# Kernel optimization log

Hardware: AMD Instinct MI355X
Metric: run time of the kernel (lower is better)

## Reference

```python
import jax, jax.numpy as jnp
import numpy as np

B, C, H, W = 8, 512, 64, 64
K = 8
NUM = K * K          # number of channel groups / graph nodes
CG = C // NUM        # channels per group (8)
NC = 19              # num_classes
OUT = 512            # bottleneck out_channels


def make_dct_weight():
    # Per-channel 2D DCT basis. Channel ch belongs to group g = ch // CG;
    # group g selects frequency (u, v) = (g % K, g // K).
    g = np.arange(C) // CG
    u = (g % K).astype(np.float64)
    v = (g // K).astype(np.float64)
    th = (np.arange(H) + 0.5) / H   # [H]
    tw = (np.arange(W) + 0.5) / W   # [W]
    bh = np.cos(np.pi * u[:, None] * th[None, :])  # [C,H]
    bw = np.cos(np.pi * v[:, None] * tw[None, :])  # [C,W]
    return (bh[:, :, None] * bw[:, None, :]).astype(np.float32)  # [C,H,W]


def setup_inputs() -> dict:
    key = jax.random.key(0)
    ks = jax.random.split(key, 10)
    s = lambda i, shape: jax.random.normal(ks[i], shape, jnp.float32) * 0.05
    return {
        'x': jax.random.normal(ks[0], (B, C, H, W), jnp.float32),
        'dct_w': jnp.asarray(make_dct_weight()),
        'dm_w1': s(1, (CG, CG)),
        'dm_gamma': jnp.ones((CG,), jnp.float32),
        'dm_beta': jnp.zeros((CG,), jnp.float32),
        'dm_w2': s(2, (NC, CG)),
        'dm_b2': s(3, (NC,)),
        'fuse_w': s(4, (NUM,)),
        'fuse_b': s(5, (1,)),
        'gcn_w1': s(6, (NUM, NUM)),
        'gcn_w2': s(7, (CG, CG)),
        'bot_w': s(8, (OUT, 2 * C, 3, 3)),
        'bot_gamma': jnp.ones((OUT,), jnp.float32),
        'bot_beta': jnp.zeros((OUT,), jnp.float32),
    }


def reference(x, dct_w, dm_w1, dm_gamma, dm_beta, dm_w2, dm_b2,
              fuse_w, fuse_b, gcn_w1, gcn_w2, bot_w, bot_gamma, bot_beta):
    # MultiSpectralDCTLayer: elementwise DCT basis multiply, keeps [B,C,H,W]
    fres = x * dct_w[None]

    # channel_split -> grouped layout [B, NUM, CG, H*W]
    xg = x.reshape(B, NUM, CG, H * W)
    fg = fres.reshape(B, NUM, CG, H * W)

    # decoder_map: 1x1 conv -> BN(eval, mean=0,var=1) -> ReLU -> (Dropout=id) -> 1x1 conv
    h1 = jnp.einsum('dc,bncp->bndp', dm_w1, fg)
    h1 = jax.nn.relu(h1 * dm_gamma[None, None, :, None] + dm_beta[None, None, :, None])
    fres_map = jnp.einsum('kc,bncp->bnkp', dm_w2, h1) + dm_b2[None, None, :, None]  # [B,n,NC,HW]

    # fuse: 1x1 conv over group dim n -> [B,NC,H,W]
    fres_map_output = (jnp.einsum('n,bnkp->bkp', fuse_w, fres_map) + fuse_b[0]).reshape(B, NC, H, W)

    # local frequency class centers: [B,n,NC,HW] @ [B,n,HW,c] -> [B,n,NC,c]
    fHWc = fg.transpose(0, 1, 3, 2)   # [B,n,HW,c]
    xHWc = xg.transpose(0, 1, 3, 2)   # [B,n,HW,c]
    local = jnp.einsum('bnkp,bnpc->bnkc', fres_map, fHWc)

    # GCN over n (node) dim: conv1 + residual ReLU, then Linear over c
    g = jnp.einsum('mn,bnkc->bmkc', gcn_w1, local)
    g = jax.nn.relu(g + local)
    local = jnp.einsum('bnkc,dc->bnkd', g, gcn_w2)

    # attention combine: softmax(x @ local^T) @ local
    wm = jax.nn.softmax(jnp.einsum('bnpc,bnkc->bnpk', xHWc, local), axis=-1)  # [B,n,HW,NC]
    out = jnp.einsum('bnpk,bnkc->bnpc', wm, local)  # [B,n,HW,c]

    # channel_recover -> [B,C,H,W]
    out = out.transpose(0, 1, 3, 2).reshape(B, C, H, W)

    # bottleneck: 3x3 conv on concat, BN(eval) affine, ReLU
    cat = jnp.concatenate([x, out], axis=1)  # [B,2C,H,W]
    y = jax.lax.conv_general_dilated(cat, bot_w, (1, 1), 'SAME',
                                     dimension_numbers=('NCHW', 'OIHW', 'NCHW'))
    y = jax.nn.relu(y * bot_gamma[None, :, None, None] + bot_beta[None, :, None, None])
    return (y, fres_map_output)
```

## Files before the change

### kernel.cpp

```cpp
#include <hip/hip_runtime.h>


typedef __attribute__((ext_vector_type(8))) unsigned short u16x8;
typedef __attribute__((ext_vector_type(8))) __bf16 bf16x8;
typedef __attribute__((ext_vector_type(4))) float f32x4;

__device__ inline unsigned short f2bf(float f) {
    unsigned int u = __float_as_uint(f);
    u += 0x7fffu + ((u >> 16) & 1u);
    return (unsigned short)(u >> 16);
}

__device__ inline float bf2f(unsigned short u) {
    return __uint_as_float(((unsigned int)u) << 16);
}

__device__ __forceinline__ void gload16(unsigned short* lds, const unsigned short* g) {
    __builtin_amdgcn_global_load_lds(
        (const __attribute__((address_space(1))) unsigned int*)g,
        (__attribute__((address_space(3))) unsigned int*)lds, 16, 0, 0);
}

__global__ __launch_bounds__(256) void dct_split(const float* __restrict__ dct,
                                                 float* __restrict__ bhw) {
    const int i = blockIdx.x * 256 + threadIdx.x;
    const int c = i >> 6;
    const int k = i & 63;
    bhw[i] = dct[(size_t)c * 4096 + k * 64];
    bhw[32768 + i] = dct[(size_t)c * 4096 + k] / dct[(size_t)c * 4096];
}

__global__ __launch_bounds__(256) void repack_w(const float* __restrict__ w,
                                                unsigned short* __restrict__ wt) {
    __shared__ float buf[9216];
    const int oc = blockIdx.x;
    const int tid = threadIdx.x;
    const float* src = w + (size_t)oc * 9216;
    for (int i = tid; i < 9216; i += 256) buf[i] = src[i];
    __syncthreads();
#pragma unroll
    for (int t = 0; t < 9; ++t) {
        for (int i = tid; i < 1024; i += 256)
            wt[((size_t)t * 512 + oc) * 1024 + i] = f2bf(buf[i * 9 + t]);
    }
}

__global__ __launch_bounds__(256) void front_kernel(
    const float* __restrict__ x, const float* __restrict__ bhw,
    const float* __restrict__ w1, const float* __restrict__ gamma,
    const float* __restrict__ beta, const float* __restrict__ w2,
    const float* __restrict__ b2, const float* __restrict__ fuse_w,
    float* __restrict__ part, float* __restrict__ fpart,
    unsigned short* __restrict__ cat) {
    __shared__ __align__(16) float fgs[8][260];
    __shared__ __align__(16) float fms[19][260];
    __shared__ float sw1[64], sw2[152], sb2[19], sg[8], sb[8], sfw[64];
    const int bid = blockIdx.x;
    const int sp = bid >> 7;
    const int b = (bid >> 4) & 7;
    const int ch = bid & 15;
    const int tid = threadIdx.x;
    if (tid < 64) { sw1[tid] = w1[tid]; sfw[tid] = fuse_w[tid]; }
    if (tid < 152) sw2[tid] = w2[tid];
    if (tid < 19) sb2[tid] = b2[tid];
    if (tid < 8) { sg[tid] = gamma[tid]; sb[tid] = beta[tid]; }
    __syncthreads();
    const int p = ch * 256 + tid;
    const int hh = p >> 6;
    const int ww = p & 63;
    const float* bhp = bhw;
    const float* bwp = bhw + 32768;
    const int kk = tid >> 3, cc = tid & 7;
    float facc[19];
#pragma unroll
    for (int k = 0; k < 19; ++k) facc[k] = 0.f;
    for (int nn = 0; nn < 16; ++nn) {
        const int n = sp * 16 + nn;
        float fg[8];
        u16x8 xw;
#pragma unroll
        for (int c = 0; c < 8; ++c) {
            const int chn = n * 8 + c;
            const float xv = x[((size_t)(b * 512 + chn)) * 4096 + p];
            fg[c] = xv * (bhp[chn * 64 + hh] * bwp[chn * 64 + ww]);
            xw[c] = f2bf(xv);
            fgs[c][tid] = fg[c];
        }
        *(u16x8*)(cat + ((size_t)(b * 4096) + p) * 1024 + n * 8) = xw;
        float h1[8];
#pragma unroll
        for (int d = 0; d < 8; ++d) {
            float s = 0.f;
#pragma unroll
            for (int c = 0; c < 8; ++c) s = fmaf(sw1[d * 8 + c], fg[c], s);
            h1[d] = fmaxf(fmaf(s, sg[d], sb[d]), 0.f);
        }
        const float fw = sfw[n];
#pragma unroll
        for (int k = 0; k < 19; ++k) {
            float s = sb2[k];
#pragma unroll
            for (int d = 0; d < 8; ++d) s = fmaf(sw2[k * 8 + d], h1[d], s);
            fms[k][tid] = s;
            facc[k] = fmaf(fw, s, facc[k]);
        }
        __syncthreads();
        if (tid < 152) {
            float accv = 0.f;
#pragma unroll 8
            for (int p4 = 0; p4 < 256; p4 += 4) {
                const float4 a = *(const float4*)&fms[kk][p4];
                const float4 g4 = *(const float4*)&fgs[cc][p4];
                accv += a.x * g4.x + a.y * g4.y + a.z * g4.z + a.w * g4.w;
            }
            part[((size_t)((b * 64 + n) * 16) + ch) * 152 + tid] = accv;
        }
        __syncthreads();
    }
#pragma unroll
    for (int k = 0; k < 19; ++k)
        fpart[((size_t)(sp * 8 + b) * 19 + k) * 4096 + p] = facc[k];
}

__global__ __launch_bounds__(256) void fuse_reduce(
    const float* __restrict__ fpart, const float* __restrict__ fuse_b,
    float* __restrict__ out1) {
    const int i = blockIdx.x * 256 + threadIdx.x;
    float s = fuse_b[0];
#pragma unroll
    for (int sp = 0; sp < 4; ++sp) s += fpart[(size_t)sp * 622592 + i];
    out1[i] = s;
}

__global__ __launch_bounds__(256) void lsum_kernel(
    const float* __restrict__ part, float* __restrict__ L) {
    const int i = blockIdx.x * 256 + threadIdx.x;
    const int bn = i / 152;
    const int t = i - bn * 152;
    float s = 0.f;
#pragma unroll
    for (int ch = 0; ch < 16; ++ch)
        s += part[((size_t)(bn * 16 + ch)) * 152 + t];
    L[i] = s;
}

__global__ __launch_bounds__(256) void gcn2_kernel(
    const float* __restrict__ Lg, const float* __restrict__ w1,
    const float* __restrict__ w2, float* __restrict__ local2) {
    __shared__ float L[9728];
    __shared__ float R[1216];
    __shared__ float sw1[4096];
    __shared__ float sw2[64];
    const int b = blockIdx.x >> 3;
    const int n0 = (blockIdx.x & 7) * 8;
    const int tid = threadIdx.x;
    for (int i = tid; i < 9728; i += 256) L[i] = Lg[(size_t)b * 9728 + i];
    for (int i = tid; i < 4096; i += 256) sw1[i] = w1[i];
    if (tid < 64) sw2[tid] = w2[tid];
    __syncthreads();
    for (int i = tid; i < 1216; i += 256) {
        const int nn = i / 152, t = i - nn * 152;
        const int m = n0 + nn;
        float g = 0.f;
        for (int n = 0; n < 64; ++n) g = fmaf(sw1[m * 64 + n], L[n * 152 + t], g);
        R[i] = fmaxf(g + L[m * 152 + t], 0.f);
    }
    __syncthreads();
    for (int i = tid; i < 1216; i += 256) {
        const int nn = i / 152, t = i - nn * 152;
        const int k = t >> 3, d = t & 7;
        float s = 0.f;
#pragma unroll
        for (int c = 0; c < 8; ++c) s = fmaf(R[nn * 152 + k * 8 + c], sw2[d * 8 + c], s);
        local2[(size_t)b * 9728 + (n0 + nn) * 152 + t] = s;
    }
}

__global__ __launch_bounds__(256) void attn_kernel(
    const float* __restrict__ local2, unsigned short* __restrict__ cat) {
    __shared__ float Ls[2432];
    const int bid = blockIdx.x;
    const int b = bid >> 6;
    const int chunk = (bid >> 2) & 15;
    const int nq = bid & 3;
    const int tid = threadIdx.x;
    for (int i = tid; i < 2432; i += 256)
        Ls[i] = local2[(size_t)b * 9728 + nq * 2432 + i];
    __syncthreads();
    const int p = chunk * 256 + tid;
    unsigned short* base = cat + ((size_t)(b * 4096) + p) * 1024;
#pragma unroll 4
    for (int nn = 0; nn < 16; ++nn) {
        const int n = nq * 16 + nn;
        const u16x8 xr = *(const u16x8*)(base + n * 8);
        float xv[8];
#pragma unroll
        for (int c = 0; c < 8; ++c) xv[c] = bf2f(xr[c]);
        const float* L = Ls + nn * 152;
        float lg[19];
        float mx = -1e30f;
#pragma unroll
        for (int k = 0; k < 19; ++k) {
            float s = 0.f;
#pragma unroll
            for (int c = 0; c < 8; ++c) s = fmaf(xv[c], L[k * 8 + c], s);
            lg[k] = s;
            mx = fmaxf(mx, s);
        }
        float se = 0.f;
#pragma unroll
        for (int k = 0; k < 19; ++k) {
            lg[k] = __expf(lg[k] - mx);
            se += lg[k];
        }
        const float inv = 1.f / se;
        float ov[8];
#pragma unroll
        for (int c = 0; c < 8; ++c) ov[c] = 0.f;
#pragma unroll
        for (int k = 0; k < 19; ++k) {
#pragma unroll
            for (int c = 0; c < 8; ++c) ov[c] = fmaf(lg[k], L[k * 8 + c], ov[c]);
        }
        u16x8 w;
#pragma unroll
        for (int c = 0; c < 8; ++c) w[c] = f2bf(ov[c] * inv);
        *(u16x8*)(base + 512 + n * 8) = w;
    }
}

__global__ __launch_bounds__(512, 1) void conv_kernel(
    const unsigned short* __restrict__ cat, const unsigned short* __restrict__ wt,
    const unsigned short* __restrict__ zp,
    const float* __restrict__ gamma, const float* __restrict__ beta,
    float* __restrict__ out) {
    __shared__ __align__(16) unsigned short As[10 * 4096];
    __shared__ __align__(16) unsigned short Bs[2 * 16384];
    const int bid0 = blockIdx.x;
    const int bid = (bid0 & 7) * 32 + (bid0 >> 3);
    const int mt = bid >> 1;
    const int nt = bid & 1;
    const int b = mt >> 4;
    const int pix0 = (mt & 15) * 256;
    const int y0 = (mt & 15) * 4;
    const int ocb = nt * 256;
    const int tid = threadIdx.x;
    const int w = tid >> 6;
    const int lane = tid & 63;
    const int l16 = lane & 15;
    const int khalf = lane >> 4;
    const int wr1 = w >> 2;
    const int wrow = wr1 * 64;
    const int wcol = (w & 3) * 32;
    const int sx = tid >> 3;
    const int icsw = ((tid & 7) ^ ((tid >> 3) & 7)) * 8;
    const unsigned short* zps = zp + icsw;
    const unsigned short* catb = cat + ((size_t)b * 4096) * 1024 + icsw;
    int colk[3][2];
#pragma unroll
    for (int d = 0; d < 3; ++d)
#pragma unroll
        for (int ks = 0; ks < 2; ++ks)
            colk[d][ks] = ((ks * 64 + khalf * 16) ^ (((l16 + d - 1) & 7) << 4)) >> 1;

    f32x4 acc[2][2][4][2];
#pragma unroll
    for (int qm = 0; qm < 2; ++qm)
#pragma unroll
        for (int qn = 0; qn < 2; ++qn)
#pragma unroll
            for (int m = 0; m < 4; ++m)
#pragma unroll
                for (int n = 0; n < 2; ++n)
#pragma unroll
                    for (int j = 0; j < 4; ++j) acc[qm][qn][m][n][j] = 0.f;

    bf16x8 af[4][2];
    bf16x8 bq[2][2];
    const bf16x8 zf = {};

#define AF_READ(QM, DY, DX)                                                        \
    {                                                                              \
        const int r_ = (QM) * 2 + wr1 + (DY) + 1;                                  \
        const int phys_ = (r_ < 2) ? r_ : r_ + 4 * cp;                             \
        const int rb_ = phys_ * 4096;                                              \
        _Pragma("unroll") for (int m_ = 0; m_ < 4; ++m_) {                         \
            const int xm_ = m_ * 16 + l16 + (DX);                                  \
            const int xc_ = ((DX) == 0) ? xm_ : min(max(xm_, 0), 63);              \
            const int ab_ = rb_ + xc_ * 64;                                        \
            _Pragma("unroll") for (int ks_ = 0; ks_ < 2; ++ks_)                    \
                af[m_][ks_] = *(const bf16x8*)(As + ab_ + colk[(DX) + 1][ks_]);    \
            if ((DX) == -1 && m_ == 0 && l16 == 0) { af[0][0] = zf; af[0][1] = zf; } \
            if ((DX) == 1 && m_ == 3 && l16 == 15) { af[3][0] = zf; af[3][1] = zf; } \
        }                                                                          \
    }

#define BQ_READ(SOFF, QN)                                                          \
    _Pragma("unroll") for (int n_ = 0; n_ < 2; ++n_)                               \
        _Pragma("unroll") for (int ks_ = 0; ks_ < 2; ++ks_)                        \
            bq[n_][ks_] = *(const bf16x8*)(Bs + (SOFF) +                           \
                ((QN) * 128 + wcol + n_ * 16 + l16) * 64 + colk[1][ks_]);

#define STAGE_BH(H, SWOFF, TAP, ICB)                                               \
    _Pragma("unroll") for (int j_ = 0; j_ < 2; ++j_) {                             \
        gload16(Bs + (SWOFF) + (H) * 8192 + (j_ * 512 + tid) * 8,                  \
                wt + (size_t)(TAP) * 524288 +                                      \
                    (size_t)(ocb + (H) * 128 + j_ * 64 + sx) * 1024 + (ICB) + icsw); \
    }

#define STAGE_AROW(R)                                                              \
    do {                                                                           \
        const int yy_ = y0 - 1 + (R);                                              \
        const int ph_ = ((R) < 2) ? (R) : (R) + 4 * cp1;                           \
        const unsigned short* s2_ = ((unsigned)yy_ < 64u)                          \
            ? catb + ((size_t)(yy_ * 64 + sx)) * 1024 + iccn : zps;                \
        gload16(As + ph_ * 4096 + tid * 8, s2_);                                   \
    } while (0)

#define MFMA_Q(QM, QN)                                                             \
    __builtin_amdgcn_s_setprio(1);                                                 \
    _Pragma("unroll") for (int m_ = 0; m_ < 4; ++m_)                               \
        _Pragma("unroll") for (int n_ = 0; n_ < 2; ++n_)                           \
            _Pragma("unroll") for (int ks_ = 0; ks_ < 2; ++ks_)                    \
                acc[QM][QN][m_][n_] = __builtin_amdgcn_mfma_f32_16x16x32_bf16(     \
                    af[m_][ks_], bq[n_][ks_], acc[QM][QN][m_][n_], 0, 0, 0);       \
    __builtin_amdgcn_s_setprio(0);

#define VWAIT(N)                                                                   \
    asm volatile("s_waitcnt vmcnt(" #N ")" ::: "memory");                          \
    __builtin_amdgcn_sched_barrier(0);

#define TAP_BODY(T, DY, DX, AROW, W0N, W2N)                                        \
    {                                                                              \
        const int s_ = (c + (T)) & 1;                                              \
        const int sr_ = s_ << 14;                                                  \
        const int sw_ = sr_ ^ 16384;                                               \
        const int tn_ = ((T) == 8) ? 0 : (T) + 1;                                  \
        const int icb_ = ((T) == 8) ? iccn : icc;                                  \
                                                                  \
        VWAIT(W0N)                                                                 \
        __builtin_amdgcn_s_barrier();                                              \
        __builtin_amdgcn_sched_barrier(0);                                         \
        AF_READ(0, DY, DX)                                                         \
        BQ_READ(sr_, 0)                                                            \
        STAGE_BH(0, sw_, tn_, icb_)                                                \
        MFMA_Q(0, 0)                                                               \
                                                                  \
        AF_READ(1, DY, DX)                                                         \
        if ((AROW) >= 0) STAGE_AROW(AROW);                                         \
        MFMA_Q(1, 0)                                                               \
                                                                  \
        VWAIT(W2N)                                                                 \
        BQ_READ(sr_, 1)                                                            \
        STAGE_BH(1, sw_, tn_, icb_)                                                \
        MFMA_Q(1, 1)                                                               \
                                                                  \
        AF_READ(0, DY, DX)                                                         \
        MFMA_Q(0, 1)                                                               \
    }

    {
        const int cp1 = 0, iccn = 0;
#pragma unroll
        for (int r = 0; r < 6; ++r) STAGE_AROW(r);
    }
    STAGE_BH(0, 0, 0, 0)
    STAGE_BH(1, 0, 0, 0)

    for (int c = 0; c < 16; ++c) {
        const int cp = c & 1;
        const int cp1 = cp ^ 1;
        const int icc = c << 6;
        const int iccn = ((c + 1) & 15) << 6;
        TAP_BODY(0, -1, -1, -1, 2, 2)
        TAP_BODY(1, -1, 0, -1, 2, 2)
        TAP_BODY(2, -1, 1, -1, 2, 2)
        TAP_BODY(3, 0, -1, 0, 2, 3)
        TAP_BODY(4, 0, 0, 2, 3, 3)
        TAP_BODY(5, 0, 1, 3, 3, 3)
        TAP_BODY(6, 1, -1, 1, 3, 3)
        TAP_BODY(7, 1, 0, 4, 3, 3)
        TAP_BODY(8, 1, 1, 5, 3, 3)
    }
    asm volatile("s_waitcnt vmcnt(0)" ::: "memory");

#pragma unroll
    for (int qn = 0; qn < 2; ++qn)
#pragma unroll
        for (int n = 0; n < 2; ++n) {
            const int oc = ocb + qn * 128 + wcol + n * 16 + l16;
            const float g = gamma[oc], bb = beta[oc];
#pragma unroll
            for (int qm = 0; qm < 2; ++qm)
#pragma unroll
                for (int m = 0; m < 4; ++m) {
                    const int P = qm * 128 + wrow + m * 16 + khalf * 4;
                    float4 o;
                    o.x = fmaxf(fmaf(acc[qm][qn][m][n][0], g, bb), 0.f);
                    o.y = fmaxf(fmaf(acc[qm][qn][m][n][1], g, bb), 0.f);
                    o.z = fmaxf(fmaf(acc[qm][qn][m][n][2], g, bb), 0.f);
                    o.w = fmaxf(fmaf(acc[qm][qn][m][n][3], g, bb), 0.f);
                    *(float4*)(out + ((size_t)(b * 512 + oc)) * 4096 + pix0 + P) = o;
                }
        }
#undef AF_READ
#undef BQ_READ
#undef STAGE_BH
#undef STAGE_AROW
#undef MFMA_Q
#undef VWAIT
#undef TAP_BODY
}

extern "C" void kernel_launch(void* const* d_in, const int* in_sizes, int n_in,
                              void* d_out, int out_size, void* d_ws, size_t ws_size,
                              hipStream_t stream) {
    const float* x = (const float*)d_in[0];
    const float* dct = (const float*)d_in[1];
    const float* dm_w1 = (const float*)d_in[2];
    const float* dm_g = (const float*)d_in[3];
    const float* dm_b = (const float*)d_in[4];
    const float* dm_w2 = (const float*)d_in[5];
    const float* dm_b2 = (const float*)d_in[6];
    const float* fuse_w = (const float*)d_in[7];
    const float* fuse_b = (const float*)d_in[8];
    const float* gcn_w1 = (const float*)d_in[9];
    const float* gcn_w2 = (const float*)d_in[10];
    const float* bot_w = (const float*)d_in[11];
    const float* bot_g = (const float*)d_in[12];
    const float* bot_b = (const float*)d_in[13];

    float* y = (float*)d_out;
    float* out1 = y + (size_t)8 * 512 * 4096;
    float* part = y;
    float* fpart = y + 1245184;
    float* Lbuf = y + 3735552;
    float* bhw = y + 3813376;

    char* ws = (char*)d_ws;
    const size_t CAT_BYTES = (size_t)8 * 4096 * 1024 * 2;
    const size_t WT_BYTES = (size_t)9 * 512 * 1024 * 2;
    const size_t PART_BYTES = (size_t)2048 * 152 * 4;
    const size_t L2_BYTES = (size_t)8 * 9728 * 4;
    const size_t ZP_BYTES = 4096;
    if (ws_size < CAT_BYTES + WT_BYTES + PART_BYTES + L2_BYTES + ZP_BYTES) return;

    unsigned short* cat = (unsigned short*)ws;
    unsigned short* wt = (unsigned short*)(ws + CAT_BYTES);
    float* local2 = (float*)(ws + CAT_BYTES + WT_BYTES + PART_BYTES);
    unsigned short* zp = (unsigned short*)(ws + CAT_BYTES + WT_BYTES + PART_BYTES + L2_BYTES);

    hipMemsetAsync(zp, 0, ZP_BYTES, stream);
    dct_split<<<dim3(128), dim3(256), 0, stream>>>(dct, bhw);
    front_kernel<<<dim3(512), dim3(256), 0, stream>>>(x, bhw, dm_w1, dm_g, dm_b,
                                                      dm_w2, dm_b2, fuse_w,
                                                      part, fpart, cat);
    lsum_kernel<<<dim3(304), dim3(256), 0, stream>>>(part, Lbuf);
    gcn2_kernel<<<dim3(64), dim3(256), 0, stream>>>(Lbuf, gcn_w1, gcn_w2, local2);
    fuse_reduce<<<dim3(2432), dim3(256), 0, stream>>>(fpart, fuse_b, out1);
    repack_w<<<dim3(512), dim3(256), 0, stream>>>(bot_w, wt);
    attn_kernel<<<dim3(512), dim3(256), 0, stream>>>(local2, cat);
    conv_kernel<<<dim3(256), dim3(512), 0, stream>>>(cat, wt, zp, bot_g, bot_b, y);
}
```

Before: 401.8 us.

## Double conv block to 1024 threads, halving per-wave output tile

Measured after the change: 777.8 us. +93.6%, slower.

```diff
diff --git a/kernel.cpp b/kernel.cpp
--- a/kernel.cpp
+++ b/kernel.cpp
@@ -229,7 +229,7 @@
     }
 }
 
-__global__ __launch_bounds__(512, 1) void conv_kernel(
+__global__ __launch_bounds__(1024, 4) void conv_kernel(
     const unsigned short* __restrict__ cat, const unsigned short* __restrict__ wt,
     const unsigned short* __restrict__ zp,
     const float* __restrict__ gamma, const float* __restrict__ beta,
@@ -249,10 +249,8 @@
     const int lane = tid & 63;
     const int l16 = lane & 15;
     const int khalf = lane >> 4;
-    const int wr1 = w >> 2;
-    const int wrow = wr1 * 64;
-    const int wcol = (w & 3) * 32;
-    const int sx = tid >> 3;
+    const int wrp = w >> 3;
+    const int wcp = w & 7;
     const int icsw = ((tid & 7) ^ ((tid >> 3) & 7)) * 8;
     const unsigned short* zps = zp + icsw;
     const unsigned short* catb = cat + ((size_t)b * 4096) * 1024 + icsw;
@@ -263,7 +261,7 @@
         for (int ks = 0; ks < 2; ++ks)
             colk[d][ks] = ((ks * 64 + khalf * 16) ^ (((l16 + d - 1) & 7) << 4)) >> 1;
 
-    f32x4 acc[2][2][4][2];
+    f32x4 acc[2][2][4];
 #pragma unroll
     for (int qm = 0; qm < 2; ++qm)
 #pragma unroll
@@ -271,17 +269,15 @@
 #pragma unroll
             for (int m = 0; m < 4; ++m)
 #pragma unroll
-                for (int n = 0; n < 2; ++n)
-#pragma unroll
-                    for (int j = 0; j < 4; ++j) acc[qm][qn][m][n][j] = 0.f;
+                for (int j = 0; j < 4; ++j) acc[qm][qn][m][j] = 0.f;
 
     bf16x8 af[4][2];
-    bf16x8 bq[2][2];
+    bf16x8 bq[2];
     const bf16x8 zf = {};
 
 #define AF_READ(QM, DY, DX)                                                        \
     {                                                                              \
-        const int r_ = (QM) * 2 + wr1 + (DY) + 1;                                  \
+        const int r_ = (QM) * 2 + wrp + (DY) + 1;                                  \
         const int phys_ = (r_ < 2) ? r_ : r_ + 4 * cp;                             \
         const int rb_ = phys_ * 4096;                                              \
         _Pragma("unroll") for (int m_ = 0; m_ < 4; ++m_) {                         \
@@ -296,41 +292,37 @@
     }
 
 #define BQ_READ(SOFF, QN)                                                          \
-    _Pragma("unroll") for (int n_ = 0; n_ < 2; ++n_)                               \
-        _Pragma("unroll") for (int ks_ = 0; ks_ < 2; ++ks_)                        \
-            bq[n_][ks_] = *(const bf16x8*)(Bs + (SOFF) +                           \
-                ((QN) * 128 + wcol + n_ * 16 + l16) * 64 + colk[1][ks_]);
+    _Pragma("unroll") for (int ks_ = 0; ks_ < 2; ++ks_)                            \
+        bq[ks_] = *(const bf16x8*)(Bs + (SOFF) +                                   \
+            ((QN) * 128 + wcp * 16 + l16) * 64 + colk[1][ks_]);
 
 #define STAGE_BH(H, SWOFF, TAP, ICB)                                               \
-    _Pragma("unroll") for (int j_ = 0; j_ < 2; ++j_) {                             \
-        gload16(Bs + (SWOFF) + (H) * 8192 + (j_ * 512 + tid) * 8,                  \
-                wt + (size_t)(TAP) * 524288 +                                      \
-                    (size_t)(ocb + (H) * 128 + j_ * 64 + sx) * 1024 + (ICB) + icsw); \
-    }
-
-#define STAGE_AROW(R)                                                              \
+    gload16(Bs + (SWOFF) + (H) * 8192 + tid * 8,                                   \
+            wt + (size_t)(TAP) * 524288 +                                          \
+                (size_t)(ocb + (H) * 128 + (tid >> 3)) * 1024 + (ICB) + icsw);
+
+#define STAGE_APAIR(R)                                                             \
     do {                                                                           \
-        const int yy_ = y0 - 1 + (R);                                              \
-        const int ph_ = ((R) < 2) ? (R) : (R) + 4 * cp1;                           \
+        const int yy_ = y0 - 1 + (R) + (tid >> 9);                                 \
+        const int slot_ = ((R) == 0) ? 0 : ((R) + 4 * cp1);                        \
         const unsigned short* s2_ = ((unsigned)yy_ < 64u)                          \
-            ? catb + ((size_t)(yy_ * 64 + sx)) * 1024 + iccn : zps;                \
-        gload16(As + ph_ * 4096 + tid * 8, s2_);                                   \
+            ? catb + ((size_t)(yy_ * 64 + ((tid >> 3) & 63))) * 1024 + iccn : zps; \
+        gload16(As + slot_ * 4096 + tid * 8, s2_);                                 \
     } while (0)
 
 #define MFMA_Q(QM, QN)                                                             \
     __builtin_amdgcn_s_setprio(1);                                                 \
     _Pragma("unroll") for (int m_ = 0; m_ < 4; ++m_)                               \
-        _Pragma("unroll") for (int n_ = 0; n_ < 2; ++n_)                           \
-            _Pragma("unroll") for (int ks_ = 0; ks_ < 2; ++ks_)                    \
-                acc[QM][QN][m_][n_] = __builtin_amdgcn_mfma_f32_16x16x32_bf16(     \
-                    af[m_][ks_], bq[n_][ks_], acc[QM][QN][m_][n_], 0, 0, 0);       \
+        _Pragma("unroll") for (int ks_ = 0; ks_ < 2; ++ks_)                        \
+            acc[QM][QN][m_] = __builtin_amdgcn_mfma_f32_16x16x32_bf16(             \
+                af[m_][ks_], bq[ks_], acc[QM][QN][m_], 0, 0, 0);                   \
     __builtin_amdgcn_s_setprio(0);
 
 #define VWAIT(N)                                                                   \
     asm volatile("s_waitcnt vmcnt(" #N ")" ::: "memory");                          \
     __builtin_amdgcn_sched_barrier(0);
 
-#define TAP_BODY(T, DY, DX, AROW, W0N, W2N)                                        \
+#define TAP_BODY(T, DY, DX, APAIR, W0N, W2N)                                       \
     {                                                                              \
         const int s_ = (c + (T)) & 1;                                              \
         const int sr_ = s_ << 14;                                                  \
@@ -347,7 +339,7 @@
         MFMA_Q(0, 0)                                                               \
                                                                   \
         AF_READ(1, DY, DX)                                                         \
-        if ((AROW) >= 0) STAGE_AROW(AROW);                                         \
+        if ((APAIR) >= 0) STAGE_APAIR(APAIR);                                      \
         MFMA_Q(1, 0)                                                               \
                                                                   \
         VWAIT(W2N)                                                                 \
@@ -356,13 +348,15 @@
         MFMA_Q(1, 1)                                                               \
                                                                   \
         AF_READ(0, DY, DX)                                                         \
+        BQ_READ(sr_, 1)                                                            \
         MFMA_Q(0, 1)                                                               \
     }
 
     {
         const int cp1 = 0, iccn = 0;
-#pragma unroll
-        for (int r = 0; r < 6; ++r) STAGE_AROW(r);
+        STAGE_APAIR(0);
+        STAGE_APAIR(2);
+        STAGE_APAIR(4);
     }
     STAGE_BH(0, 0, 0, 0)
     STAGE_BH(1, 0, 0, 0)
@@ -372,41 +366,39 @@
         const int cp1 = cp ^ 1;
         const int icc = c << 6;
         const int iccn = ((c + 1) & 15) << 6;
-        TAP_BODY(0, -1, -1, -1, 2, 2)
-        TAP_BODY(1, -1, 0, -1, 2, 2)
-        TAP_BODY(2, -1, 1, -1, 2, 2)
-        TAP_BODY(3, 0, -1, 0, 2, 3)
-        TAP_BODY(4, 0, 0, 2, 3, 3)
-        TAP_BODY(5, 0, 1, 3, 3, 3)
-        TAP_BODY(6, 1, -1, 1, 3, 3)
-        TAP_BODY(7, 1, 0, 4, 3, 3)
-        TAP_BODY(8, 1, 1, 5, 3, 3)
+        TAP_BODY(0, -1, -1, -1, 1, 1)
+        TAP_BODY(1, -1, 0, -1, 1, 1)
+        TAP_BODY(2, -1, 1, -1, 1, 1)
+        TAP_BODY(3, 0, -1, 2, 1, 2)
+        TAP_BODY(4, 0, 0, 4, 2, 2)
+        TAP_BODY(5, 0, 1, -1, 2, 1)
+        TAP_BODY(6, 1, -1, 0, 1, 2)
+        TAP_BODY(7, 1, 0, -1, 2, 1)
+        TAP_BODY(8, 1, 1, -1, 1, 1)
     }
     asm volatile("s_waitcnt vmcnt(0)" ::: "memory");
 
 #pragma unroll
-    for (int qn = 0; qn < 2; ++qn)
-#pragma unroll
-        for (int n = 0; n < 2; ++n) {
-            const int oc = ocb + qn * 128 + wcol + n * 16 + l16;
-            const float g = gamma[oc], bb = beta[oc];
-#pragma unroll
-            for (int qm = 0; qm < 2; ++qm)
-#pragma unroll
-                for (int m = 0; m < 4; ++m) {
-                    const int P = qm * 128 + wrow + m * 16 + khalf * 4;
-                    float4 o;
-                    o.x = fmaxf(fmaf(acc[qm][qn][m][n][0], g, bb), 0.f);
-                    o.y = fmaxf(fmaf(acc[qm][qn][m][n][1], g, bb), 0.f);
-                    o.z = fmaxf(fmaf(acc[qm][qn][m][n][2], g, bb), 0.f);
-                    o.w = fmaxf(fmaf(acc[qm][qn][m][n][3], g, bb), 0.f);
-                    *(float4*)(out + ((size_t)(b * 512 + oc)) * 4096 + pix0 + P) = o;
-                }
-        }
+    for (int qn = 0; qn < 2; ++qn) {
+        const int oc = ocb + qn * 128 + wcp * 16 + l16;
+        const float g = gamma[oc], bb = beta[oc];
+#pragma unroll
+        for (int qm = 0; qm < 2; ++qm)
+#pragma unroll
+            for (int m = 0; m < 4; ++m) {
+                const int P = qm * 128 + wrp * 64 + m * 16 + khalf * 4;
+                float4 o;
+                o.x = fmaxf(fmaf(acc[qm][qn][m][0], g, bb), 0.f);
+                o.y = fmaxf(fmaf(acc[qm][qn][m][1], g, bb), 0.f);
+                o.z = fmaxf(fmaf(acc[qm][qn][m][2], g, bb), 0.f);
+                o.w = fmaxf(fmaf(acc[qm][qn][m][3], g, bb), 0.f);
+                *(float4*)(out + ((size_t)(b * 512 + oc)) * 4096 + pix0 + P) = o;
+            }
+    }
 #undef AF_READ
 #undef BQ_READ
 #undef STAGE_BH
-#undef STAGE_AROW
+#undef STAGE_APAIR
 #undef MFMA_Q
 #undef VWAIT
 #undef TAP_BODY
@@ -460,5 +452,5 @@
     fuse_reduce<<<dim3(2432), dim3(256), 0, stream>>>(fpart, fuse_b, out1);
     repack_w<<<dim3(512), dim3(256), 0, stream>>>(bot_w, wt);
     attn_kernel<<<dim3(512), dim3(256), 0, stream>>>(local2, cat);
-    conv_kernel<<<dim3(256), dim3(512), 0, stream>>>(cat, wt, zp, bot_g, bot_b, y);
-}
+    conv_kernel<<<dim3(256), dim3(1024), 0, stream>>>(cat, wt, zp, bot_g, bot_b, y);
+}
```
